# Kernel optimization log

Hardware: AMD Instinct MI355X
Metric: run time of the kernel (lower is better)

## Reference

```python
import jax, jax.numpy as jnp
import numpy as np

D_K = 64
SCALE = D_K ** (-0.5)
B, H, S = 2, 16, 2048


def setup_inputs() -> dict:
    key = jax.random.key(0)
    kq, kk, kv = jax.random.split(key, 3)
    q = jax.random.normal(kq, (B, H, S, D_K), dtype=jnp.float32)
    k = jax.random.normal(kk, (B, H, S, D_K), dtype=jnp.float32)
    v = jax.random.normal(kv, (B, H, S, D_K), dtype=jnp.float32)
    # causal mask: True means masked (matches torch masked_fill semantics)
    mask = jnp.triu(jnp.ones((S, S), dtype=bool), k=1)[None, None]  # [1,1,S,S]
    return {"q": q, "k": k, "v": v, "mask": mask}


def reference(q, k, v, mask) -> jnp.ndarray:
    # scores = q @ k^T  -> [B,H,S,S]
    scores = jnp.einsum("bhqd,bhkd->bhqk", q, k)
    # masked_fill(mask, -inf), then scale (as written in the source),
    # then softmax over the key axis. -inf * scale stays -inf.
    scores = jnp.where(mask, -jnp.inf, scores)
    attn = jax.nn.softmax(SCALE * scores, axis=-1)
    return jnp.einsum("bhqk,bhkd->bhqd", attn, v)
```

## Files before the change

### kernel.cpp

```cpp
#include <hip/hip_runtime.h>
#include <hip/hip_bf16.h>
#include <math.h>


constexpr int S  = 2048;
constexpr int D  = 64;
constexpr int BH = 32;
constexpr float SCALE = 0.125f;
constexpr float LOG2E = 1.4426950408889634f;
constexpr float QPRE  = SCALE * LOG2E;
constexpr int PSTR = 72;

typedef __attribute__((ext_vector_type(8))) short bf16x8;
typedef __attribute__((ext_vector_type(4))) short bf16x4;
typedef __attribute__((ext_vector_type(4))) float f32x4;

#if __has_builtin(__builtin_amdgcn_mfma_f32_16x16x16bf16_1k)
#define HAS_MFMA_1K 1
#else
#define HAS_MFMA_1K 0
#endif

#if __has_builtin(__builtin_amdgcn_exp2f)
#define EXP2F(x) __builtin_amdgcn_exp2f(x)
#else
#define EXP2F(x) exp2f(x)
#endif

__device__ __forceinline__ short f2bf(float x) {
    union { __hip_bfloat16 b; short s; } u; u.b = __float2bfloat16(x); return u.s;
}

__device__ __forceinline__ void gload_lds16(const void* g, void* lds) {
    __builtin_amdgcn_global_load_lds(
        (const __attribute__((address_space(1))) unsigned int*)g,
        (__attribute__((address_space(3))) unsigned int*)lds, 16, 0, 0);
}

__global__ __launch_bounds__(256) void preconv_25993142075924(
    const float* __restrict__ Kg, const float* __restrict__ Vg,
    short* __restrict__ Kb, short* __restrict__ VT)
{
    const int kt = blockIdx.x, bh = blockIdx.y, tid = threadIdx.x;
    __shared__ float lt[64 * 65];
    const float* kp = Kg + (size_t)bh * S * D;
    const float* vp = Vg + (size_t)bh * S * D;
    short* kb = Kb + (size_t)bh * S * D;
    short* vt = VT + (size_t)bh * D * S;
    #pragma unroll
    for (int e = 0; e < 4; ++e) {
        int idx = (tid + e * 256) * 4;
        int r = idx >> 6, c = idx & 63;
        f32x4 k4 = *(const f32x4*)(kp + (size_t)(kt * 64 + r) * D + c);
        bf16x4 kb4;
        kb4[0] = f2bf(k4[0]); kb4[1] = f2bf(k4[1]);
        kb4[2] = f2bf(k4[2]); kb4[3] = f2bf(k4[3]);
        *(bf16x4*)(kb + (size_t)(kt * 64 + r) * D + c) = kb4;
        f32x4 v4 = *(const f32x4*)(vp + (size_t)(kt * 64 + r) * D + c);
        lt[(c + 0) * 65 + r] = v4[0];
        lt[(c + 1) * 65 + r] = v4[1];
        lt[(c + 2) * 65 + r] = v4[2];
        lt[(c + 3) * 65 + r] = v4[3];
    }
    __syncthreads();
    #pragma unroll
    for (int e = 0; e < 2; ++e) {
        int tt = tid + e * 256;
        int d  = tt >> 3;
        int j0 = (tt & 7) * 8;
        bf16x8 o;
        #pragma unroll
        for (int jj = 0; jj < 8; ++jj)
            o[jj] = f2bf(lt[d * 65 + j0 + jj]);
        *(bf16x8*)(vt + (size_t)d * S + kt * 64 + j0) = o;
    }
}

__global__ __launch_bounds__(256, 4) void attn_fwd_v11_25993142075924(
    const float* __restrict__ Qg, const short* __restrict__ Kb,
    const short* __restrict__ VT, float* __restrict__ Og)
{
    const int bh  = blockIdx.x;
    const int yy  = blockIdx.y;
    const int a   = yy & 7;
    const int b   = yy >> 3;
    const int qb  = (b == 0) ? a : (b == 1) ? 15 - a : (b == 2) ? 16 + a : 31 - a;
    const int tid = threadIdx.x;
    const int wv  = tid >> 6;
    const int ln  = tid & 63;
    const int c16 = ln & 15;
    const int qd  = ln >> 4;

    const int q0  = qb * 64 + wv * 16;
    const int nkt = qb + 1;

    __shared__ __align__(16) short lk[3][64 * 64];
    __shared__ __align__(16) short lv[2][64 * 64];
#if !HAS_MFMA_1K
    __shared__ __align__(16) short lp[4 * 16 * PSTR];
    short* lpw = lp + wv * 16 * PSTR;
#endif

    const float* qp = Qg + (size_t)bh * S * D;
    const short* kp = Kb + (size_t)bh * S * D;
    const short* vp = VT + (size_t)bh * D * S;
    float*       op = Og + (size_t)bh * S * D;

    const int srow0 = wv * 16 + (ln >> 3);
    const int sgrp0 = (ln & 7) ^ (srow0 & 7);
    const int srow1 = srow0 + 8;
    const int sgrp1 = (ln & 7) ^ (srow1 & 7);

    bf16x8 qf[2];
    {
        const float* src = qp + (size_t)(q0 + c16) * D + qd * 8;
        #pragma unroll
        for (int khf = 0; khf < 2; ++khf) {
            f32x4 aa = *(const f32x4*)(src + khf * 32);
            f32x4 bb = *(const f32x4*)(src + khf * 32 + 4);
            bf16x8 f;
            f[0] = f2bf(aa[0] * QPRE); f[1] = f2bf(aa[1] * QPRE);
            f[2] = f2bf(aa[2] * QPRE); f[3] = f2bf(aa[3] * QPRE);
            f[4] = f2bf(bb[0] * QPRE); f[5] = f2bf(bb[1] * QPRE);
            f[6] = f2bf(bb[2] * QPRE); f[7] = f2bf(bb[3] * QPRE);
            qf[khf] = f;
        }
    }

    f32x4 oacc[4] = {{0,0,0,0},{0,0,0,0},{0,0,0,0},{0,0,0,0}};
    float lsum = 0.f;

    #define STAGE_K(t, buf)                                                        \
        do {                                                                       \
            gload_lds16(kp + ((size_t)(t) * 64 + srow0) * D + sgrp0 * 8,           \
                        &lk[buf][(wv * 16 + 0) * 64]);                             \
            gload_lds16(kp + ((size_t)(t) * 64 + srow1) * D + sgrp1 * 8,           \
                        &lk[buf][(wv * 16 + 8) * 64]);                             \
        } while (0)
    #define STAGE_V(t, buf)                                                        \
        do {                                                                       \
            gload_lds16(vp + (size_t)srow0 * S + (t) * 64 + sgrp0 * 8,             \
                        &lv[buf][(wv * 16 + 0) * 64]);                             \
            gload_lds16(vp + (size_t)srow1 * S + (t) * 64 + sgrp1 * 8,             \
                        &lv[buf][(wv * 16 + 8) * 64]);                             \
        } while (0)

    STAGE_K(0, 0);
    STAGE_V(0, 0);
    if (nkt > 1) {
        STAGE_K(1, 1);
        asm volatile("s_waitcnt vmcnt(2)" ::: "memory");
    } else {
        asm volatile("s_waitcnt vmcnt(0)" ::: "memory");
    }
    __builtin_amdgcn_s_barrier();

    int kcur = 0, kst = 2;
    for (int kt = 0; kt < nkt; ++kt) {
        const int vcur = kt & 1;
        if (kt + 1 < nkt) STAGE_V(kt + 1, vcur ^ 1);
        if (kt + 2 < nkt) STAGE_K(kt + 2, kst);

#if HAS_MFMA_1K
        bf16x4 vf[4][4];
        #pragma unroll
        for (int dt = 0; dt < 4; ++dt) {
            const int row = dt * 16 + c16;
            #pragma unroll
            for (int nt = 0; nt < 4; ++nt) {
                const int gl = nt * 2 + (qd >> 1);
                const int gp = gl ^ (c16 & 7);
                vf[dt][nt] = *(const bf16x4*)&lv[vcur][row * 64 + gp * 8 + (qd & 1) * 4];
            }
        }
#endif

        float t[4][4];
        __builtin_amdgcn_s_setprio(1);
        #pragma unroll
        for (int nt = 0; nt < 4; ++nt) {
            const int row = nt * 16 + c16;
            f32x4 acc = {0,0,0,0};
            #pragma unroll
            for (int khf = 0; khf < 2; ++khf) {
                const int g = (khf * 4 + qd) ^ (row & 7);
                bf16x8 kf = *(const bf16x8*)&lk[kcur][row * 64 + g * 8];
                acc = __builtin_amdgcn_mfma_f32_16x16x32_bf16(kf, qf[khf], acc, 0, 0, 0);
            }
            t[nt][0] = acc[0]; t[nt][1] = acc[1]; t[nt][2] = acc[2]; t[nt][3] = acc[3];
        }
        __builtin_amdgcn_s_setprio(0);

        if (kt == qb) {
            #pragma unroll
            for (int nt = 0; nt < 4; ++nt) {
                #pragma unroll
                for (int r = 0; r < 4; ++r) {
                    int key = kt * 64 + nt * 16 + qd * 4 + r;
                    if (key > q0 + c16) t[nt][r] = -INFINITY;
                }
            }
        }

        float pval[4][4];
        #pragma unroll
        for (int nt = 0; nt < 4; ++nt)
            #pragma unroll
            for (int r = 0; r < 4; ++r) {
                float pv = EXP2F(t[nt][r]);
                pval[nt][r] = pv;
                lsum += pv;
            }

#if HAS_MFMA_1K
        __builtin_amdgcn_s_setprio(1);
        #pragma unroll
        for (int nt = 0; nt < 4; ++nt) {
            bf16x4 pf;
            pf[0] = f2bf(pval[nt][0]); pf[1] = f2bf(pval[nt][1]);
            pf[2] = f2bf(pval[nt][2]); pf[3] = f2bf(pval[nt][3]);
            #pragma unroll
            for (int dt = 0; dt < 4; ++dt)
                oacc[dt] = __builtin_amdgcn_mfma_f32_16x16x16bf16_1k(
                    vf[dt][nt], pf, oacc[dt], 0, 0, 0);
        }
        __builtin_amdgcn_s_setprio(0);
#else
        #pragma unroll
        for (int nt = 0; nt < 4; ++nt)
            #pragma unroll
            for (int r = 0; r < 4; ++r)
                lpw[c16 * PSTR + nt * 16 + qd * 4 + r] = f2bf(pval[nt][r]);
        bf16x8 pf2[2];
        #pragma unroll
        for (int khf = 0; khf < 2; ++khf)
            pf2[khf] = *(const bf16x8*)&lpw[c16 * PSTR + khf * 32 + qd * 8];
        #pragma unroll
        for (int dt = 0; dt < 4; ++dt) {
            const int row = dt * 16 + c16;
            #pragma unroll
            for (int khf = 0; khf < 2; ++khf) {
                const int g = (khf * 4 + qd) ^ (row & 7);
                bf16x8 vf8 = *(const bf16x8*)&lv[vcur][row * 64 + g * 8];
                oacc[dt] = __builtin_amdgcn_mfma_f32_16x16x32_bf16(vf8, pf2[khf], oacc[dt], 0, 0, 0);
            }
        }
#endif

        if (kt + 2 < nkt) {
            asm volatile("s_waitcnt vmcnt(2)" ::: "memory");
            __builtin_amdgcn_s_barrier();
        } else if (kt + 1 < nkt) {
            asm volatile("s_waitcnt vmcnt(0)" ::: "memory");
            __builtin_amdgcn_s_barrier();
        }
        kcur = (kcur == 2) ? 0 : kcur + 1;
        kst  = (kst  == 2) ? 0 : kst  + 1;
    }
    #undef STAGE_K
    #undef STAGE_V

    float s = lsum;
    s += __shfl_xor(s, 16);
    s += __shfl_xor(s, 32);
    const float inv = 1.0f / s;
    float* dst = op + (size_t)(q0 + c16) * D;
    #pragma unroll
    for (int dt = 0; dt < 4; ++dt) {
        f32x4 o;
        o[0] = oacc[dt][0] * inv; o[1] = oacc[dt][1] * inv;
        o[2] = oacc[dt][2] * inv; o[3] = oacc[dt][3] * inv;
        *(f32x4*)(dst + dt * 16 + qd * 4) = o;
    }
}

__global__ __launch_bounds__(256) void attn_fwd_v1_25993142075924(
    const float* __restrict__ Qg, const float* __restrict__ Kg,
    const float* __restrict__ Vg, float* __restrict__ Og)
{
    constexpr int KSTR = 72;
    constexpr int BQ = 64, BK = 64;
    const int qt  = blockIdx.x;
    const int bh  = blockIdx.y;
    const int tid = threadIdx.x;
    const int wv  = tid >> 6;
    const int ln  = tid & 63;
    const int c16 = ln & 15;
    const int qd  = ln >> 4;

    __shared__ __align__(16) __hip_bfloat16 lk [BK][KSTR];
    __shared__ __align__(16) __hip_bfloat16 lvt[D ][KSTR];
    __shared__ __align__(16) __hip_bfloat16 lp [4][16][KSTR];

    const size_t hoff = (size_t)bh * S * D;
    const float* qp = Qg + hoff;
    const float* kp = Kg + hoff;
    const float* vp = Vg + hoff;
    float*       op = Og + hoff;
    const int q0 = qt * BQ;

    bf16x8 qf[2];
    {
        const float* src = qp + (size_t)(q0 + wv*16 + c16) * D + qd*8;
        #pragma unroll
        for (int kh = 0; kh < 2; ++kh) {
            f32x4 a = *(const f32x4*)(src + kh*32);
            f32x4 b = *(const f32x4*)(src + kh*32 + 4);
            bf16x8 f;
            f[0]=f2bf(a[0]*QPRE); f[1]=f2bf(a[1]*QPRE); f[2]=f2bf(a[2]*QPRE); f[3]=f2bf(a[3]*QPRE);
            f[4]=f2bf(b[0]*QPRE); f[5]=f2bf(b[1]*QPRE); f[6]=f2bf(b[2]*QPRE); f[7]=f2bf(b[3]*QPRE);
            qf[kh] = f;
        }
    }

    f32x4 oacc[4] = {{0,0,0,0},{0,0,0,0},{0,0,0,0},{0,0,0,0}};
    float mrun[4] = {-INFINITY,-INFINITY,-INFINITY,-INFINITY};
    float lrun[4] = {0.f,0.f,0.f,0.f};

    const int nkt = qt + 1;
    for (int kt = 0; kt < nkt; ++kt) {
        __syncthreads();
        #pragma unroll
        for (int e = 0; e < 4; ++e) {
            int idx = (tid + e*256) * 4;
            int row = idx >> 6, col = idx & 63;
            f32x4 k4 = *(const f32x4*)(kp + (size_t)(kt*BK + row)*D + col);
            bf16x4 kb;
            kb[0]=f2bf(k4[0]); kb[1]=f2bf(k4[1]); kb[2]=f2bf(k4[2]); kb[3]=f2bf(k4[3]);
            *(bf16x4*)&lk[row][col] = kb;
            f32x4 v4 = *(const f32x4*)(vp + (size_t)(kt*BK + row)*D + col);
            lvt[col+0][row] = __float2bfloat16(v4[0]);
            lvt[col+1][row] = __float2bfloat16(v4[1]);
            lvt[col+2][row] = __float2bfloat16(v4[2]);
            lvt[col+3][row] = __float2bfloat16(v4[3]);
        }
        __syncthreads();

        float t[4][4];
        #pragma unroll
        for (int nt = 0; nt < 4; ++nt) {
            f32x4 acc = {0,0,0,0};
            #pragma unroll
            for (int kh = 0; kh < 2; ++kh) {
                bf16x8 kf = *(const bf16x8*)&lk[nt*16 + c16][kh*32 + qd*8];
                acc = __builtin_amdgcn_mfma_f32_16x16x32_bf16(qf[kh], kf, acc, 0, 0, 0);
            }
            #pragma unroll
            for (int r = 0; r < 4; ++r) t[nt][r] = acc[r];
        }
        if (kt == nkt - 1) {
            #pragma unroll
            for (int nt = 0; nt < 4; ++nt) {
                int j = kt*BK + nt*16 + c16;
                #pragma unroll
                for (int r = 0; r < 4; ++r)
                    if (j > q0 + wv*16 + qd*4 + r) t[nt][r] = -INFINITY;
            }
        }

        float pval[4][4];
        #pragma unroll
        for (int r = 0; r < 4; ++r) {
            float tm = fmaxf(fmaxf(t[0][r], t[1][r]), fmaxf(t[2][r], t[3][r]));
            tm = fmaxf(tm, __shfl_xor(tm, 1));
            tm = fmaxf(tm, __shfl_xor(tm, 2));
            tm = fmaxf(tm, __shfl_xor(tm, 4));
            tm = fmaxf(tm, __shfl_xor(tm, 8));
            float mnew  = fmaxf(mrun[r], tm);
            float alpha = exp2f(mrun[r] - mnew);
            mrun[r] = mnew;
            float rs = 0.f;
            #pragma unroll
            for (int nt = 0; nt < 4; ++nt) {
                float pv = exp2f(t[nt][r] - mnew);
                pval[nt][r] = pv;
                rs += pv;
            }
            rs += __shfl_xor(rs, 1);
            rs += __shfl_xor(rs, 2);
            rs += __shfl_xor(rs, 4);
            rs += __shfl_xor(rs, 8);
            lrun[r] = lrun[r] * alpha + rs;
            #pragma unroll
            for (int dt = 0; dt < 4; ++dt) oacc[dt][r] *= alpha;
        }

        #pragma unroll
        for (int nt = 0; nt < 4; ++nt)
            #pragma unroll
            for (int r = 0; r < 4; ++r)
                lp[wv][qd*4 + r][nt*16 + c16] = __float2bfloat16(pval[nt][r]);
        bf16x8 pf[2];
        #pragma unroll
        for (int kh = 0; kh < 2; ++kh)
            pf[kh] = *(const bf16x8*)&lp[wv][c16][kh*32 + qd*8];

        #pragma unroll
        for (int dt = 0; dt < 4; ++dt) {
            #pragma unroll
            for (int kh = 0; kh < 2; ++kh) {
                bf16x8 vf = *(const bf16x8*)&lvt[dt*16 + c16][kh*32 + qd*8];
                oacc[dt] = __builtin_amdgcn_mfma_f32_16x16x32_bf16(pf[kh], vf, oacc[dt], 0, 0, 0);
            }
        }
    }

    #pragma unroll
    for (int r = 0; r < 4; ++r) {
        float inv = 1.0f / lrun[r];
        float* dst = op + (size_t)(q0 + wv*16 + qd*4 + r) * D;
        #pragma unroll
        for (int dt = 0; dt < 4; ++dt)
            dst[dt*16 + c16] = oacc[dt][r] * inv;
    }
}

extern "C" void kernel_launch(void* const* d_in, const int* in_sizes, int n_in,
                              void* d_out, int out_size, void* d_ws, size_t ws_size,
                              hipStream_t stream) {
    const float* q = (const float*)d_in[0];
    const float* k = (const float*)d_in[1];
    const float* v = (const float*)d_in[2];
    float* out = (float*)d_out;
    const size_t elems = (size_t)BH * S * D;
    const size_t need  = 2 * elems * sizeof(short);
    if (ws_size >= need) {
        short* Kb = (short*)d_ws;
        short* VT = Kb + elems;
        preconv_25993142075924<<<dim3(S / 64, BH), 256, 0, stream>>>(k, v, Kb, VT);
        attn_fwd_v11_25993142075924<<<dim3(BH, 32), 256, 0, stream>>>(q, Kb, VT, out);
    } else {
        attn_fwd_v1_25993142075924<<<dim3(S / 64, BH), 256, 0, stream>>>(q, k, v, out);
    }
}
```

Baseline: 141.9 us.

## Use persistent atomic work queue with longest-first causal tile scheduling

Replaces the fixed grid of query-block tiles with a work-stealing loop. Each block pulls items from a global atomic counter, which the preconversion kernel resets, and items are ordered so the longest causal rows (highest qb) run first. The aim is better load balance across CUs for the triangular causal workload. In exchange it adds an atomic plus two block barriers per item. The grid is still 1024 blocks, the same as the item count, so blocks mostly take one item each and the gain comes from dynamic ordering rather than true persistence.

```diff
diff --git a/kernel.cpp b/kernel.cpp
--- a/kernel.cpp
+++ b/kernel.cpp
@@ -10,6 +10,7 @@
 constexpr float LOG2E = 1.4426950408889634f;
 constexpr float QPRE  = SCALE * LOG2E;
 constexpr int PSTR = 72;
+constexpr int NITEMS = BH * 32;
 
 typedef __attribute__((ext_vector_type(8))) short bf16x8;
 typedef __attribute__((ext_vector_type(4))) short bf16x4;
@@ -39,9 +40,11 @@
 
 __global__ __launch_bounds__(256) void preconv_25993142075924(
     const float* __restrict__ Kg, const float* __restrict__ Vg,
-    short* __restrict__ Kb, short* __restrict__ VT)
+    short* __restrict__ Kb, short* __restrict__ VT,
+    unsigned int* __restrict__ ctr)
 {
     const int kt = blockIdx.x, bh = blockIdx.y, tid = threadIdx.x;
+    if (kt == 0 && bh == 0 && tid == 0) atomicExch(ctr, 0u);
     __shared__ float lt[64 * 65];
     const float* kp = Kg + (size_t)bh * S * D;
     const float* vp = Vg + (size_t)bh * S * D;
@@ -76,59 +79,29 @@
     }
 }
 
-__global__ __launch_bounds__(256, 4) void attn_fwd_v11_25993142075924(
+__global__ __launch_bounds__(256, 4) void attn_fwd_v13_25993142075924(
     const float* __restrict__ Qg, const short* __restrict__ Kb,
-    const short* __restrict__ VT, float* __restrict__ Og)
+    const short* __restrict__ VT, float* __restrict__ Og,
+    unsigned int* __restrict__ ctr)
 {
-    const int bh  = blockIdx.x;
-    const int yy  = blockIdx.y;
-    const int a   = yy & 7;
-    const int b   = yy >> 3;
-    const int qb  = (b == 0) ? a : (b == 1) ? 15 - a : (b == 2) ? 16 + a : 31 - a;
     const int tid = threadIdx.x;
     const int wv  = tid >> 6;
     const int ln  = tid & 63;
     const int c16 = ln & 15;
     const int qd  = ln >> 4;
 
-    const int q0  = qb * 64 + wv * 16;
-    const int nkt = qb + 1;
-
     __shared__ __align__(16) short lk[3][64 * 64];
     __shared__ __align__(16) short lv[2][64 * 64];
+    __shared__ int s_item;
 #if !HAS_MFMA_1K
     __shared__ __align__(16) short lp[4 * 16 * PSTR];
     short* lpw = lp + wv * 16 * PSTR;
 #endif
 
-    const float* qp = Qg + (size_t)bh * S * D;
-    const short* kp = Kb + (size_t)bh * S * D;
-    const short* vp = VT + (size_t)bh * D * S;
-    float*       op = Og + (size_t)bh * S * D;
-
     const int srow0 = wv * 16 + (ln >> 3);
     const int sgrp0 = (ln & 7) ^ (srow0 & 7);
     const int srow1 = srow0 + 8;
     const int sgrp1 = (ln & 7) ^ (srow1 & 7);
-
-    bf16x8 qf[2];
-    {
-        const float* src = qp + (size_t)(q0 + c16) * D + qd * 8;
-        #pragma unroll
-        for (int khf = 0; khf < 2; ++khf) {
-            f32x4 aa = *(const f32x4*)(src + khf * 32);
-            f32x4 bb = *(const f32x4*)(src + khf * 32 + 4);
-            bf16x8 f;
-            f[0] = f2bf(aa[0] * QPRE); f[1] = f2bf(aa[1] * QPRE);
-            f[2] = f2bf(aa[2] * QPRE); f[3] = f2bf(aa[3] * QPRE);
-            f[4] = f2bf(bb[0] * QPRE); f[5] = f2bf(bb[1] * QPRE);
-            f[6] = f2bf(bb[2] * QPRE); f[7] = f2bf(bb[3] * QPRE);
-            qf[khf] = f;
-        }
-    }
-
-    f32x4 oacc[4] = {{0,0,0,0},{0,0,0,0},{0,0,0,0},{0,0,0,0}};
-    float lsum = 0.f;
 
     #define STAGE_K(t, buf)                                                        \
         do {                                                                       \
@@ -145,133 +118,171 @@
                         &lv[buf][(wv * 16 + 8) * 64]);                             \
         } while (0)
 
-    STAGE_K(0, 0);
-    STAGE_V(0, 0);
-    if (nkt > 1) {
-        STAGE_K(1, 1);
-        asm volatile("s_waitcnt vmcnt(2)" ::: "memory");
-    } else {
-        asm volatile("s_waitcnt vmcnt(0)" ::: "memory");
-    }
-    __builtin_amdgcn_s_barrier();
-
-    int kcur = 0, kst = 2;
-    for (int kt = 0; kt < nkt; ++kt) {
-        const int vcur = kt & 1;
-        if (kt + 1 < nkt) STAGE_V(kt + 1, vcur ^ 1);
-        if (kt + 2 < nkt) STAGE_K(kt + 2, kst);
+    for (;;) {
+        if (tid == 0) s_item = (int)atomicAdd(ctr, 1u);
+        __syncthreads();
+        const int item = s_item;
+        __syncthreads();
+        if (item >= NITEMS) break;
+
+        const int qb = 31 - (item >> 5);
+        const int bh = item & 31;
+
+        const int q0  = qb * 64 + wv * 16;
+        const int nkt = qb + 1;
+
+        const float* qp = Qg + (size_t)bh * S * D;
+        const short* kp = Kb + (size_t)bh * S * D;
+        const short* vp = VT + (size_t)bh * D * S;
+        float*       op = Og + (size_t)bh * S * D;
+
+        bf16x8 qf[2];
+        {
+            const float* src = qp + (size_t)(q0 + c16) * D + qd * 8;
+            #pragma unroll
+            for (int khf = 0; khf < 2; ++khf) {
+                f32x4 aa = *(const f32x4*)(src + khf * 32);
+                f32x4 bb = *(const f32x4*)(src + khf * 32 + 4);
+                bf16x8 f;
+                f[0] = f2bf(aa[0] * QPRE); f[1] = f2bf(aa[1] * QPRE);
+                f[2] = f2bf(aa[2] * QPRE); f[3] = f2bf(aa[3] * QPRE);
+                f[4] = f2bf(bb[0] * QPRE); f[5] = f2bf(bb[1] * QPRE);
+                f[6] = f2bf(bb[2] * QPRE); f[7] = f2bf(bb[3] * QPRE);
+                qf[khf] = f;
+            }
+        }
+
+        f32x4 oacc[4] = {{0,0,0,0},{0,0,0,0},{0,0,0,0},{0,0,0,0}};
+        float lsum = 0.f;
+
+        STAGE_K(0, 0);
+        STAGE_V(0, 0);
+        if (nkt > 1) {
+            STAGE_K(1, 1);
+            asm volatile("s_waitcnt vmcnt(2)" ::: "memory");
+        } else {
+            asm volatile("s_waitcnt vmcnt(0)" ::: "memory");
+        }
+        __builtin_amdgcn_s_barrier();
+
+        int kcur = 0, kst = 2;
+        for (int kt = 0; kt < nkt; ++kt) {
+            const int vcur = kt & 1;
+            if (kt + 1 < nkt) STAGE_V(kt + 1, vcur ^ 1);
+            if (kt + 2 < nkt) STAGE_K(kt + 2, kst);
 
 #if HAS_MFMA_1K
-        bf16x4 vf[4][4];
+            bf16x4 vf[4][4];
+            #pragma unroll
+            for (int dt = 0; dt < 4; ++dt) {
+                const int row = dt * 16 + c16;
+                #pragma unroll
+                for (int nt = 0; nt < 4; ++nt) {
+                    const int gl = nt * 2 + (qd >> 1);
+                    const int gp = gl ^ (c16 & 7);
+                    vf[dt][nt] = *(const bf16x4*)&lv[vcur][row * 64 + gp * 8 + (qd & 1) * 4];
+                }
+            }
+#endif
+
+            float t[4][4];
+            __builtin_amdgcn_s_setprio(1);
+            #pragma unroll
+            for (int nt = 0; nt < 4; ++nt) {
+                const int row = nt * 16 + c16;
+                f32x4 acc = {0,0,0,0};
+                #pragma unroll
+                for (int khf = 0; khf < 2; ++khf) {
+                    const int g = (khf * 4 + qd) ^ (row & 7);
+                    bf16x8 kf = *(const bf16x8*)&lk[kcur][row * 64 + g * 8];
+                    acc = __builtin_amdgcn_mfma_f32_16x16x32_bf16(kf, qf[khf], acc, 0, 0, 0);
+                }
+                t[nt][0] = acc[0]; t[nt][1] = acc[1]; t[nt][2] = acc[2]; t[nt][3] = acc[3];
+            }
+            __builtin_amdgcn_s_setprio(0);
+
+            if (kt == qb) {
+                #pragma unroll
+                for (int nt = 0; nt < 4; ++nt) {
+                    #pragma unroll
+                    for (int r = 0; r < 4; ++r) {
+                        int key = kt * 64 + nt * 16 + qd * 4 + r;
+                        if (key > q0 + c16) t[nt][r] = -INFINITY;
+                    }
+                }
+            }
+
+            float pval[4][4];
+            #pragma unroll
+            for (int nt = 0; nt < 4; ++nt)
+                #pragma unroll
+                for (int r = 0; r < 4; ++r) {
+                    float pv = EXP2F(t[nt][r]);
+                    pval[nt][r] = pv;
+                    lsum += pv;
+                }
+
+#if HAS_MFMA_1K
+            __builtin_amdgcn_s_setprio(1);
+            #pragma unroll
+            for (int nt = 0; nt < 4; ++nt) {
+                bf16x4 pf;
+                pf[0] = f2bf(pval[nt][0]); pf[1] = f2bf(pval[nt][1]);
+                pf[2] = f2bf(pval[nt][2]); pf[3] = f2bf(pval[nt][3]);
+                #pragma unroll
+                for (int dt = 0; dt < 4; ++dt)
+                    oacc[dt] = __builtin_amdgcn_mfma_f32_16x16x16bf16_1k(
+                        vf[dt][nt], pf, oacc[dt], 0, 0, 0);
+            }
+            __builtin_amdgcn_s_setprio(0);
+#else
+            #pragma unroll
+            for (int nt = 0; nt < 4; ++nt)
+                #pragma unroll
+                for (int r = 0; r < 4; ++r)
+                    lpw[c16 * PSTR + nt * 16 + qd * 4 + r] = f2bf(pval[nt][r]);
+            bf16x8 pf2[2];
+            #pragma unroll
+            for (int khf = 0; khf < 2; ++khf)
+                pf2[khf] = *(const bf16x8*)&lpw[c16 * PSTR + khf * 32 + qd * 8];
+            #pragma unroll
+            for (int dt = 0; dt < 4; ++dt) {
+                const int row = dt * 16 + c16;
+                #pragma unroll
+                for (int khf = 0; khf < 2; ++khf) {
+                    const int g = (khf * 4 + qd) ^ (row & 7);
+                    bf16x8 vf8 = *(const bf16x8*)&lv[vcur][row * 64 + g * 8];
+                    oacc[dt] = __builtin_amdgcn_mfma_f32_16x16x32_bf16(vf8, pf2[khf], oacc[dt], 0, 0, 0);
+                }
+            }
+#endif
+
+            if (kt + 2 < nkt) {
+                asm volatile("s_waitcnt vmcnt(2)" ::: "memory");
+                __builtin_amdgcn_s_barrier();
+            } else if (kt + 1 < nkt) {
+                asm volatile("s_waitcnt vmcnt(0)" ::: "memory");
+                __builtin_amdgcn_s_barrier();
+            }
+            kcur = (kcur == 2) ? 0 : kcur + 1;
+            kst  = (kst  == 2) ? 0 : kst  + 1;
+        }
+
+        float s2 = lsum;
+        s2 += __shfl_xor(s2, 16);
+        s2 += __shfl_xor(s2, 32);
+        const float inv = 1.0f / s2;
+        float* dst = op + (size_t)(q0 + c16) * D;
         #pragma unroll
         for (int dt = 0; dt < 4; ++dt) {
-            const int row = dt * 16 + c16;
-            #pragma unroll
-            for (int nt = 0; nt < 4; ++nt) {
-                const int gl = nt * 2 + (qd >> 1);
-                const int gp = gl ^ (c16 & 7);
-                vf[dt][nt] = *(const bf16x4*)&lv[vcur][row * 64 + gp * 8 + (qd & 1) * 4];
-            }
-        }
-#endif
-
-        float t[4][4];
-        __builtin_amdgcn_s_setprio(1);
-        #pragma unroll
-        for (int nt = 0; nt < 4; ++nt) {
-            const int row = nt * 16 + c16;
-            f32x4 acc = {0,0,0,0};
-            #pragma unroll
-            for (int khf = 0; khf < 2; ++khf) {
-                const int g = (khf * 4 + qd) ^ (row & 7);
-                bf16x8 kf = *(const bf16x8*)&lk[kcur][row * 64 + g * 8];
-                acc = __builtin_amdgcn_mfma_f32_16x16x32_bf16(kf, qf[khf], acc, 0, 0, 0);
-            }
-            t[nt][0] = acc[0]; t[nt][1] = acc[1]; t[nt][2] = acc[2]; t[nt][3] = acc[3];
-        }
-        __builtin_amdgcn_s_setprio(0);
-
-        if (kt == qb) {
-            #pragma unroll
-            for (int nt = 0; nt < 4; ++nt) {
-                #pragma unroll
-                for (int r = 0; r < 4; ++r) {
-                    int key = kt * 64 + nt * 16 + qd * 4 + r;
-                    if (key > q0 + c16) t[nt][r] = -INFINITY;
-                }
-            }
-        }
-
-        float pval[4][4];
-        #pragma unroll
-        for (int nt = 0; nt < 4; ++nt)
-            #pragma unroll
-            for (int r = 0; r < 4; ++r) {
-                float pv = EXP2F(t[nt][r]);
-                pval[nt][r] = pv;
-                lsum += pv;
-            }
-
-#if HAS_MFMA_1K
-        __builtin_amdgcn_s_setprio(1);
-        #pragma unroll
-        for (int nt = 0; nt < 4; ++nt) {
-            bf16x4 pf;
-            pf[0] = f2bf(pval[nt][0]); pf[1] = f2bf(pval[nt][1]);
-            pf[2] = f2bf(pval[nt][2]); pf[3] = f2bf(pval[nt][3]);
-            #pragma unroll
-            for (int dt = 0; dt < 4; ++dt)
-                oacc[dt] = __builtin_amdgcn_mfma_f32_16x16x16bf16_1k(
-                    vf[dt][nt], pf, oacc[dt], 0, 0, 0);
-        }
-        __builtin_amdgcn_s_setprio(0);
-#else
-        #pragma unroll
-        for (int nt = 0; nt < 4; ++nt)
-            #pragma unroll
-            for (int r = 0; r < 4; ++r)
-                lpw[c16 * PSTR + nt * 16 + qd * 4 + r] = f2bf(pval[nt][r]);
-        bf16x8 pf2[2];
-        #pragma unroll
-        for (int khf = 0; khf < 2; ++khf)
-            pf2[khf] = *(const bf16x8*)&lpw[c16 * PSTR + khf * 32 + qd * 8];
-        #pragma unroll
-        for (int dt = 0; dt < 4; ++dt) {
-            const int row = dt * 16 + c16;
-            #pragma unroll
-            for (int khf = 0; khf < 2; ++khf) {
-                const int g = (khf * 4 + qd) ^ (row & 7);
-                bf16x8 vf8 = *(const bf16x8*)&lv[vcur][row * 64 + g * 8];
-                oacc[dt] = __builtin_amdgcn_mfma_f32_16x16x32_bf16(vf8, pf2[khf], oacc[dt], 0, 0, 0);
-            }
-        }
-#endif
-
-        if (kt + 2 < nkt) {
-            asm volatile("s_waitcnt vmcnt(2)" ::: "memory");
-            __builtin_amdgcn_s_barrier();
-        } else if (kt + 1 < nkt) {
-            asm volatile("s_waitcnt vmcnt(0)" ::: "memory");
-            __builtin_amdgcn_s_barrier();
-        }
-        kcur = (kcur == 2) ? 0 : kcur + 1;
-        kst  = (kst  == 2) ? 0 : kst  + 1;
+            f32x4 o;
+            o[0] = oacc[dt][0] * inv; o[1] = oacc[dt][1] * inv;
+            o[2] = oacc[dt][2] * inv; o[3] = oacc[dt][3] * inv;
+            *(f32x4*)(dst + dt * 16 + qd * 4) = o;
+        }
     }
     #undef STAGE_K
     #undef STAGE_V
-
-    float s = lsum;
-    s += __shfl_xor(s, 16);
-    s += __shfl_xor(s, 32);
-    const float inv = 1.0f / s;
-    float* dst = op + (size_t)(q0 + c16) * D;
-    #pragma unroll
-    for (int dt = 0; dt < 4; ++dt) {
-        f32x4 o;
-        o[0] = oacc[dt][0] * inv; o[1] = oacc[dt][1] * inv;
-        o[2] = oacc[dt][2] * inv; o[3] = oacc[dt][3] * inv;
-        *(f32x4*)(dst + dt * 16 + qd * 4) = o;
-    }
 }
 
 __global__ __launch_bounds__(256) void attn_fwd_v1_25993142075924(
@@ -423,12 +434,13 @@
     const float* v = (const float*)d_in[2];
     float* out = (float*)d_out;
     const size_t elems = (size_t)BH * S * D;
-    const size_t need  = 2 * elems * sizeof(short);
+    const size_t need  = 2 * elems * sizeof(short) + sizeof(unsigned int);
     if (ws_size >= need) {
         short* Kb = (short*)d_ws;
         short* VT = Kb + elems;
-        preconv_25993142075924<<<dim3(S / 64, BH), 256, 0, stream>>>(k, v, Kb, VT);
-        attn_fwd_v11_25993142075924<<<dim3(BH, 32), 256, 0, stream>>>(q, Kb, VT, out);
+        unsigned int* ctr = (unsigned int*)(VT + elems);
+        preconv_25993142075924<<<dim3(S / 64, BH), 256, 0, stream>>>(k, v, Kb, VT, ctr);
+        attn_fwd_v13_25993142075924<<<dim3(1024), 256, 0, stream>>>(q, Kb, VT, out, ctr);
     } else {
         attn_fwd_v1_25993142075924<<<dim3(S / 64, BH), 256, 0, stream>>>(q, k, v, out);
     }
```

After: 152.6 us. 7.5% more time.
